# Kernel optimization log

Hardware: AMD Instinct MI355X
Metric: run time of the kernel (lower is better)

## Reference

```python
import jax, jax.numpy as jnp
import numpy as np

N_NODES = 50000
N_EDGES = 400000
H = 64          # node hidden state dim (entities_dimensions['node'])
E_DIM = 8       # edge_params dim (message.extra_parameters)
MSG_HID = 128   # message-creation MLP hidden width
RD_HID = 128    # readout hidden width
T = 2           # message-passing steps


def setup_inputs() -> dict:
    key = jax.random.key(0)
    ks = jax.random.split(key, 12)
    def w(k, shape):
        return jax.random.normal(k, shape, dtype=jnp.float32) * 0.05
    return {
        "node_feats": jax.random.normal(ks[0], (N_NODES, H), dtype=jnp.float32),
        "edge_feats": jax.random.normal(ks[1], (N_EDGES, E_DIM), dtype=jnp.float32),
        "edge_src": jax.random.randint(ks[2], (N_EDGES,), 0, N_NODES),
        "edge_dst": jax.random.randint(ks[3], (N_EDGES,), 0, N_NODES),
        # message creation MLP: concat(hs_src, hs_dst, edge_params) -> relu -> H
        "W_msg1": w(ks[4], (2 * H + E_DIM, MSG_HID)),
        "b_msg1": jnp.zeros((MSG_HID,), jnp.float32),
        "W_msg2": w(ks[5], (MSG_HID, H)),
        "b_msg2": jnp.zeros((H,), jnp.float32),
        # GRU cell update (keras GRUCell convention, reset_after=False)
        "W_x": w(ks[6], (H, 3 * H)),
        "W_h": w(ks[7], (H, 3 * H)),
        "b_gru": jnp.zeros((3 * H,), jnp.float32),
        # readout MLP: H -> relu -> 1
        "W_r1": w(ks[8], (H, RD_HID)),
        "b_r1": jnp.zeros((RD_HID,), jnp.float32),
        "W_r2": w(ks[9], (RD_HID, 1)),
        "b_r2": jnp.zeros((1,), jnp.float32),
    }


def _gru_cell(h, x, W_x, W_h, b):
    # gates order: update (z), reset (r), candidate (h~) — keras convention
    gx = x @ W_x + b
    gh = h @ W_h
    xz, xr, xh = jnp.split(gx, 3, axis=-1)
    hz, hr, hh = jnp.split(gh, 3, axis=-1)
    z = jax.nn.sigmoid(xz + hz)
    r = jax.nn.sigmoid(xr + hr)
    hc = jnp.tanh(xh + r * hh)
    return z * h + (1.0 - z) * hc


def reference(node_feats, edge_feats, edge_src, edge_dst,
              W_msg1, b_msg1, W_msg2, b_msg2,
              W_x, W_h, b_gru, W_r1, b_r1, W_r2, b_r2):
    h = node_feats  # [N, H] hidden states initialized from entity features
    for _ in range(T):
        # gather source/destination node states per edge: [E, H]
        src_h = h[edge_src]
        dst_h = h[edge_dst]
        m_in = jnp.concatenate([src_h, dst_h, edge_feats], axis=-1)  # [E, 2H+E_DIM]
        m = jax.nn.relu(m_in @ W_msg1 + b_msg1) @ W_msg2 + b_msg2    # [E, H]
        # scatter-sum aggregation to destination nodes: [N, H]
        agg = jax.ops.segment_sum(m, edge_dst, num_segments=N_NODES)
        # recurrent (GRU) node-state update
        h = _gru_cell(h, agg, W_x, W_h, b_gru)
    # readout MLP on final hidden states
    out = jax.nn.relu(h @ W_r1 + b_r1) @ W_r2 + b_r2  # [N, 1]
    return out
```

## Files before the change

kernel.cpp:

```cpp
#include <hip/hip_runtime.h>
#include <hip/hip_bf16.h>

#define NN 50000
#define NE 400000
#define NPAIR 12500
#define NCH 196
#define NPAD 50176

typedef __bf16 bf16_t;
typedef __bf16 bf16x4 __attribute__((ext_vector_type(4)));
typedef __bf16 bf16x8 __attribute__((ext_vector_type(8)));
typedef float  floatx4 __attribute__((ext_vector_type(4)));

static __device__ __forceinline__ floatx4 mfma16(bf16x8 a, bf16x8 b, floatx4 c) {
    return __builtin_amdgcn_mfma_f32_16x16x32_bf16(a, b, c, 0, 0, 0);
}
static __device__ __forceinline__ float sigm_f(float x) {
    return 1.f / (1.f + __expf(-x));
}
static __device__ __forceinline__ float tanh_f(float x) {
    return 1.f - 2.f / (__expf(2.f * x) + 1.f);
}
static __device__ __forceinline__ bf16x8 cvt8(const float* sp) {
    float4 f0 = *(const float4*)sp;
    float4 f1 = *(const float4*)(sp + 4);
    bf16x8 v;
    v[0] = (bf16_t)f0.x; v[1] = (bf16_t)f0.y; v[2] = (bf16_t)f0.z; v[3] = (bf16_t)f0.w;
    v[4] = (bf16_t)f1.x; v[5] = (bf16_t)f1.y; v[6] = (bf16_t)f1.z; v[7] = (bf16_t)f1.w;
    return v;
}

__global__ __launch_bounds__(256) void prep_kernel(
    const float* __restrict__ nf,
    const float* __restrict__ Wm1, const float* __restrict__ Wm2,
    const float* __restrict__ Wx,  const float* __restrict__ Wh,
    const float* __restrict__ Wr1,
    bf16_t* __restrict__ hb,
    bf16_t* __restrict__ W1f, bf16_t* __restrict__ W2f,
    bf16_t* __restrict__ Wxt, bf16_t* __restrict__ Wht,
    bf16_t* __restrict__ Wr1f)
{
    int u = blockIdx.x * 256 + threadIdx.x;
    if (u < 800000) {
        float4 v = *(const float4*)(nf + (size_t)u * 4);
        bf16x4 o;
        o[0] = (bf16_t)v.x; o[1] = (bf16_t)v.y; o[2] = (bf16_t)v.z; o[3] = (bf16_t)v.w;
        *(bf16x4*)(hb + (size_t)u * 4) = o;
        return;
    }
    u -= 800000;
    if (u < 20480) {
        int j = u & 7, l = (u >> 3) & 63, rem = u >> 9;
        int ks = rem % 5, nt = rem / 5;
        int n = nt * 16 + (l & 15);
        int k = ks * 32 + (l >> 4) * 8 + j;
        W1f[u] = (k < 136) ? (bf16_t)Wm1[k * 128 + n] : (bf16_t)0.f;
        return;
    }
    u -= 20480;
    if (u < 8192) {
        int j = u & 7, l = (u >> 3) & 63, rem = u >> 9;
        int kg = rem & 3, nt = rem >> 2;
        int n = nt * 16 + (l & 15);
        int k = kg * 32 + (l >> 4) * 8 + j;
        W2f[u] = (bf16_t)Wm2[k * 64 + n];
        return;
    }
    u -= 8192;
    if (u < 12288) {
        int n = u >> 6, k = u & 63;
        Wxt[u] = (bf16_t)Wx[k * 192 + n];
        return;
    }
    u -= 12288;
    if (u < 12288) {
        int n = u >> 6, k = u & 63;
        Wht[u] = (bf16_t)Wh[k * 192 + n];
        return;
    }
    u -= 12288;
    if (u < 8192) {
        int j = u & 7, l = (u >> 3) & 63, rem = u >> 9;
        int kg = rem & 1, nt = rem >> 1;
        int n = nt * 16 + (l & 15);
        int k = kg * 32 + (l >> 4) * 8 + j;
        Wr1f[u] = (bf16_t)Wr1[k * 128 + n];
    }
}

__global__ __launch_bounds__(256) void hist_kernel(
    const int* __restrict__ edst, int* __restrict__ deg)
{
    int e = blockIdx.x * 256 + threadIdx.x;
    if (e < NE) atomicAdd(&deg[edst[e]], 1);
}

__global__ __launch_bounds__(256) void scanA_kernel(
    const int* __restrict__ deg, int* __restrict__ chunkSums)
{
    __shared__ int s[256];
    int i = blockIdx.x * 256 + threadIdx.x;
    s[threadIdx.x] = deg[i];
    __syncthreads();
    for (int st = 128; st >= 1; st >>= 1) {
        if (threadIdx.x < st) s[threadIdx.x] += s[threadIdx.x + st];
        __syncthreads();
    }
    if (threadIdx.x == 0) chunkSums[blockIdx.x] = s[0];
}

__global__ __launch_bounds__(256) void scanB_kernel(
    const int* __restrict__ chunkSums, int* __restrict__ chunkOff)
{
    __shared__ int s[256];
    int t = threadIdx.x;
    int v = (t < NCH) ? chunkSums[t] : 0;
    s[t] = v;
    __syncthreads();
    for (int st = 1; st < 256; st <<= 1) {
        int add = (t >= st) ? s[t - st] : 0;
        __syncthreads();
        s[t] += add;
        __syncthreads();
    }
    if (t < NCH) chunkOff[t] = s[t] - v;
}

__global__ __launch_bounds__(256) void scanC_kernel(
    const int* __restrict__ deg, const int* __restrict__ chunkOff,
    int* __restrict__ cursor)
{
    __shared__ int s[256];
    int t = threadIdx.x;
    int i = blockIdx.x * 256 + t;
    int v = deg[i];
    s[t] = v;
    __syncthreads();
    for (int st = 1; st < 256; st <<= 1) {
        int add = (t >= st) ? s[t - st] : 0;
        __syncthreads();
        s[t] += add;
        __syncthreads();
    }
    cursor[i] = chunkOff[blockIdx.x] + s[t] - v;
}

__global__ __launch_bounds__(256) void scatter_kernel(
    const int* __restrict__ esrc, const int* __restrict__ edst,
    const float* __restrict__ ef,
    int* __restrict__ cursor, int* __restrict__ srcs, int* __restrict__ dsts,
    bf16_t* __restrict__ efpb)
{
    int e = blockIdx.x * 256 + threadIdx.x;
    if (e >= NE) return;
    int d = edst[e];
    int p = atomicAdd(&cursor[d], 1);
    srcs[p] = esrc[e];
    dsts[p] = d;
    float4 a = *(const float4*)(ef + (size_t)e * 8);
    float4 b = *(const float4*)(ef + (size_t)e * 8 + 4);
    bf16x8 v;
    v[0] = (bf16_t)a.x; v[1] = (bf16_t)a.y; v[2] = (bf16_t)a.z; v[3] = (bf16_t)a.w;
    v[4] = (bf16_t)b.x; v[5] = (bf16_t)b.y; v[6] = (bf16_t)b.z; v[7] = (bf16_t)b.w;
    *(bf16x8*)(efpb + (size_t)p * 8) = v;
}

__global__ __launch_bounds__(256) void edge_kernel(
    const bf16_t* __restrict__ hb, const bf16_t* __restrict__ efpb,
    const int* __restrict__ srcs, const int* __restrict__ dsts,
    const bf16_t* __restrict__ W1f, const bf16_t* __restrict__ W2f,
    const float* __restrict__ b1f, const float* __restrict__ b2f,
    bf16_t* __restrict__ mb)
{
    __shared__ __attribute__((aligned(16))) bf16_t w1s[20480];
    __shared__ __attribute__((aligned(16))) bf16_t w2s[8192];
    __shared__ __attribute__((aligned(16))) bf16_t hq[4][32 * 36];

    const int tid = threadIdx.x;
    {
        const uint4* s1 = (const uint4*)W1f;
        uint4* d1 = (uint4*)w1s;
        #pragma unroll
        for (int i = 0; i < 10; i++) d1[tid + i * 256] = s1[tid + i * 256];
        const uint4* s2 = (const uint4*)W2f;
        uint4* d2 = (uint4*)w2s;
        #pragma unroll
        for (int i = 0; i < 4; i++) d2[tid + i * 256] = s2[tid + i * 256];
    }
    __syncthreads();

    const int lane = tid & 63;
    const int wv   = tid >> 6;
    const int l15  = lane & 15;
    const int quad = lane >> 4;

    float b1r[8], b2r[4];
    #pragma unroll
    for (int nt = 0; nt < 8; nt++) b1r[nt] = b1f[nt * 16 + l15];
    #pragma unroll
    for (int nt = 0; nt < 4; nt++) b2r[nt] = b2f[nt * 16 + l15];

    const int WTOT = gridDim.x * 4;
    int p = blockIdx.x * 4 + wv;

    bf16x8 af0[5], af1[5];
    {
        int base = p * 32;
        int r0 = base + l15, r1 = base + 16 + l15;
        int si0 = srcs[r0], di0 = dsts[r0];
        int si1 = srcs[r1], di1 = dsts[r1];
        const bf16_t* sp0 = hb + (size_t)si0 * 64 + quad * 8;
        const bf16_t* dp0 = hb + (size_t)di0 * 64 + quad * 8;
        const bf16_t* sp1 = hb + (size_t)si1 * 64 + quad * 8;
        const bf16_t* dp1 = hb + (size_t)di1 * 64 + quad * 8;
        af0[0] = *(const bf16x8*)sp0;  af0[1] = *(const bf16x8*)(sp0 + 32);
        af0[2] = *(const bf16x8*)dp0;  af0[3] = *(const bf16x8*)(dp0 + 32);
        af1[0] = *(const bf16x8*)sp1;  af1[1] = *(const bf16x8*)(sp1 + 32);
        af1[2] = *(const bf16x8*)dp1;  af1[3] = *(const bf16x8*)(dp1 + 32);
        if (quad == 0) {
            af0[4] = *(const bf16x8*)(efpb + (size_t)r0 * 8);
            af1[4] = *(const bf16x8*)(efpb + (size_t)r1 * 8);
        } else {
            #pragma unroll
            for (int q = 0; q < 8; q++) { af0[4][q] = (bf16_t)0.f; af1[4][q] = (bf16_t)0.f; }
        }
    }

    while (true) {
        int pn = p + WTOT;
        int pp = (pn < NPAIR) ? pn : p;
        int nbase = pp * 32;
        int nr0 = nbase + l15, nr1 = nbase + 16 + l15;
        int si0n = srcs[nr0], di0n = dsts[nr0];
        int si1n = srcs[nr1], di1n = dsts[nr1];

        floatx4 oa0[4], oa1[4];
        #pragma unroll
        for (int nt = 0; nt < 4; nt++) {
            oa0[nt].x=0.f; oa0[nt].y=0.f; oa0[nt].z=0.f; oa0[nt].w=0.f;
            oa1[nt].x=0.f; oa1[nt].y=0.f; oa1[nt].z=0.f; oa1[nt].w=0.f;
        }

        #pragma unroll
        for (int q = 0; q < 4; q++) {
            floatx4 ac0[2], ac1[2];
            #pragma unroll
            for (int nt = 0; nt < 2; nt++) {
                ac0[nt].x=0.f; ac0[nt].y=0.f; ac0[nt].z=0.f; ac0[nt].w=0.f;
                ac1[nt].x=0.f; ac1[nt].y=0.f; ac1[nt].z=0.f; ac1[nt].w=0.f;
            }
            #pragma unroll
            for (int nt = 0; nt < 2; nt++) {
                int gnt = q * 2 + nt;
                #pragma unroll
                for (int ks = 0; ks < 5; ks++) {
                    bf16x8 b = *(const bf16x8*)(w1s + ((gnt * 5 + ks) * 64 + lane) * 8);
                    ac0[nt] = mfma16(af0[ks], b, ac0[nt]);
                    ac1[nt] = mfma16(af1[ks], b, ac1[nt]);
                }
            }
            #pragma unroll
            for (int nt = 0; nt < 2; nt++) {
                float bb = b1r[q * 2 + nt];
                #pragma unroll
                for (int r = 0; r < 4; r++) {
                    float v0 = fmaxf(ac0[nt][r] + bb, 0.f);
                    float v1 = fmaxf(ac1[nt][r] + bb, 0.f);
                    hq[wv][(quad * 4 + r) * 36 + nt * 16 + l15]      = (bf16_t)v0;
                    hq[wv][(16 + quad * 4 + r) * 36 + nt * 16 + l15] = (bf16_t)v1;
                }
            }
            bf16x8 hf0 = *(const bf16x8*)(hq[wv] + l15 * 36 + quad * 8);
            bf16x8 hf1 = *(const bf16x8*)(hq[wv] + (16 + l15) * 36 + quad * 8);
            #pragma unroll
            for (int nt = 0; nt < 4; nt++) {
                bf16x8 w2 = *(const bf16x8*)(w2s + ((nt * 4 + q) * 64 + lane) * 8);
                oa0[nt] = mfma16(hf0, w2, oa0[nt]);
                oa1[nt] = mfma16(hf1, w2, oa1[nt]);
            }
        }

        int base = p * 32;
        {
            const bf16_t* sp0 = hb + (size_t)si0n * 64 + quad * 8;
            const bf16_t* dp0 = hb + (size_t)di0n * 64 + quad * 8;
            const bf16_t* sp1 = hb + (size_t)si1n * 64 + quad * 8;
            const bf16_t* dp1 = hb + (size_t)di1n * 64 + quad * 8;
            af0[0] = *(const bf16x8*)sp0;  af0[1] = *(const bf16x8*)(sp0 + 32);
            af0[2] = *(const bf16x8*)dp0;  af0[3] = *(const bf16x8*)(dp0 + 32);
            af1[0] = *(const bf16x8*)sp1;  af1[1] = *(const bf16x8*)(sp1 + 32);
            af1[2] = *(const bf16x8*)dp1;  af1[3] = *(const bf16x8*)(dp1 + 32);
            if (quad == 0) {
                af0[4] = *(const bf16x8*)(efpb + (size_t)nr0 * 8);
                af1[4] = *(const bf16x8*)(efpb + (size_t)nr1 * 8);
            }
        }

        #pragma unroll
        for (int nt = 0; nt < 4; nt++) {
            int col = nt * 16 + l15;
            float bb = b2r[nt];
            #pragma unroll
            for (int r = 0; r < 4; r++) {
                int row0 = base + quad * 4 + r;
                int row1 = base + 16 + quad * 4 + r;
                mb[(size_t)row0 * 64 + col] = (bf16_t)(oa0[nt][r] + bb);
                mb[(size_t)row1 * 64 + col] = (bf16_t)(oa1[nt][r] + bb);
            }
        }

        if (pn >= NPAIR) break;
        p = pn;
    }
}

__global__ __launch_bounds__(256) void agg_kernel(
    const bf16_t* __restrict__ mb, const int* __restrict__ deg,
    const int* __restrict__ cursor, bf16_t* __restrict__ aggb)
{
    const int node = blockIdx.x * 4 + (threadIdx.x >> 6);
    if (node >= NN) return;
    const int lane = threadIdx.x & 63;
    int dg  = deg[node];
    int end = cursor[node];
    int st  = end - dg;
    float s0 = 0.f, s1 = 0.f;
    int e = st;
    for (; e + 1 < end; e += 2) {
        s0 += (float)mb[(size_t)e * 64 + lane];
        s1 += (float)mb[(size_t)(e + 1) * 64 + lane];
    }
    if (e < end) s0 += (float)mb[(size_t)e * 64 + lane];
    aggb[(size_t)node * 64 + lane] = (bf16_t)(s0 + s1);
}

template<int LAST>
__global__ __launch_bounds__(256) void gru_kernel(
    const bf16_t* __restrict__ aggb, const float* __restrict__ h_in,
    float* __restrict__ h_out, bf16_t* __restrict__ hb_out,
    const bf16_t* __restrict__ Wxt, const bf16_t* __restrict__ Wht,
    const float* __restrict__ bg,
    const bf16_t* __restrict__ Wr1f, const float* __restrict__ br1,
    const float* __restrict__ Wr2, const float* __restrict__ br2,
    float* __restrict__ out)
{
    __shared__ __attribute__((aligned(16))) float  shd[64 * 68];
    __shared__ __attribute__((aligned(16))) bf16_t hb2[4][16 * 72];
    const int tid = threadIdx.x;
    const int n0  = blockIdx.x * 64;

    for (int idx = tid; idx < 64 * 16; idx += 256) {
        int i = idx >> 4, c = (idx & 15) * 4;
        int n = n0 + i; if (n >= NN) n = NN - 1;
        *(float4*)&shd[i * 68 + c] = *(const float4*)(h_in + (size_t)n * 64 + c);
    }
    __syncthreads();

    const int lane = tid & 63;
    const int wv   = tid >> 6;
    const int l15  = lane & 15;
    const int quad = lane >> 4;
    const int rowA = wv * 16 + l15;
    int nA = n0 + rowA; if (nA >= NN) nA = NN - 1;

    bf16x8 ax[2], ah[2];
    ax[0] = *(const bf16x8*)(aggb + (size_t)nA * 64 + quad * 8);
    ax[1] = *(const bf16x8*)(aggb + (size_t)nA * 64 + quad * 8 + 32);
    {
        const float* hp = shd + rowA * 68 + quad * 8;
        ah[0] = cvt8(hp);
        ah[1] = cvt8(hp + 32);
    }

    floatx4 az[4], ar[4], axh[4], ahh[4];
    #pragma unroll
    for (int nt = 0; nt < 4; nt++) {
        az[nt].x=0.f; az[nt].y=0.f; az[nt].z=0.f; az[nt].w=0.f;
        ar[nt].x=0.f; ar[nt].y=0.f; ar[nt].z=0.f; ar[nt].w=0.f;
        axh[nt].x=0.f; axh[nt].y=0.f; axh[nt].z=0.f; axh[nt].w=0.f;
        ahh[nt].x=0.f; ahh[nt].y=0.f; ahh[nt].z=0.f; ahh[nt].w=0.f;
    }
    #pragma unroll
    for (int nt = 0; nt < 4; nt++) {
        const bf16_t* bx_z = Wxt + (nt * 16 + l15) * 64 + quad * 8;
        const bf16_t* bh_z = Wht + (nt * 16 + l15) * 64 + quad * 8;
        const bf16_t* bx_r = bx_z + 64 * 64;
        const bf16_t* bh_r = bh_z + 64 * 64;
        const bf16_t* bx_h = bx_z + 128 * 64;
        const bf16_t* bh_h = bh_z + 128 * 64;
        az[nt]  = mfma16(ax[0], *(const bf16x8*)bx_z,        az[nt]);
        az[nt]  = mfma16(ax[1], *(const bf16x8*)(bx_z + 32), az[nt]);
        az[nt]  = mfma16(ah[0], *(const bf16x8*)bh_z,        az[nt]);
        az[nt]  = mfma16(ah[1], *(const bf16x8*)(bh_z + 32), az[nt]);
        ar[nt]  = mfma16(ax[0], *(const bf16x8*)bx_r,        ar[nt]);
        ar[nt]  = mfma16(ax[1], *(const bf16x8*)(bx_r + 32), ar[nt]);
        ar[nt]  = mfma16(ah[0], *(const bf16x8*)bh_r,        ar[nt]);
        ar[nt]  = mfma16(ah[1], *(const bf16x8*)(bh_r + 32), ar[nt]);
        axh[nt] = mfma16(ax[0], *(const bf16x8*)bx_h,        axh[nt]);
        axh[nt] = mfma16(ax[1], *(const bf16x8*)(bx_h + 32), axh[nt]);
        ahh[nt] = mfma16(ah[0], *(const bf16x8*)bh_h,        ahh[nt]);
        ahh[nt] = mfma16(ah[1], *(const bf16x8*)(bh_h + 32), ahh[nt]);
    }

    #pragma unroll
    for (int nt = 0; nt < 4; nt++) {
        int j = nt * 16 + l15;
        float bz = bg[j], brr = bg[64 + j], bh = bg[128 + j];
        #pragma unroll
        for (int r = 0; r < 4; r++) {
            int lrow = wv * 16 + quad * 4 + r;
            int n = n0 + lrow;
            float z  = sigm_f(az[nt][r] + bz);
            float rr = sigm_f(ar[nt][r] + brr);
            float hc = tanh_f(axh[nt][r] + bh + rr * ahh[nt][r]);
            float hold = shd[lrow * 68 + j];
            float hnew = z * hold + (1.f - z) * hc;
            if (LAST) {
                hb2[wv][(quad * 4 + r) * 72 + j] = (bf16_t)hnew;
            } else if (n < NN) {
                h_out[(size_t)n * 64 + j]  = hnew;
                hb_out[(size_t)n * 64 + j] = (bf16_t)hnew;
            }
        }
    }

    if (LAST) {
        bf16x8 a0 = *(const bf16x8*)(hb2[wv] + l15 * 72 + quad * 8);
        bf16x8 a1 = *(const bf16x8*)(hb2[wv] + l15 * 72 + quad * 8 + 32);
        floatx4 accR[8];
        #pragma unroll
        for (int nt = 0; nt < 8; nt++) { accR[nt].x=0.f; accR[nt].y=0.f; accR[nt].z=0.f; accR[nt].w=0.f; }
        #pragma unroll
        for (int nt = 0; nt < 8; nt++) {
            bf16x8 b0 = *(const bf16x8*)(Wr1f + ((nt * 2 + 0) * 64 + lane) * 8);
            bf16x8 b1 = *(const bf16x8*)(Wr1f + ((nt * 2 + 1) * 64 + lane) * 8);
            accR[nt] = mfma16(a0, b0, accR[nt]);
            accR[nt] = mfma16(a1, b1, accR[nt]);
        }
        float br1r[8], wr2r[8];
        #pragma unroll
        for (int nt = 0; nt < 8; nt++) {
            br1r[nt] = br1[nt * 16 + l15];
            wr2r[nt] = Wr2[nt * 16 + l15];
        }
        float br2v = br2[0];
        #pragma unroll
        for (int r = 0; r < 4; r++) {
            float p = 0.f;
            #pragma unroll
            for (int nt = 0; nt < 8; nt++)
                p += fmaxf(accR[nt][r] + br1r[nt], 0.f) * wr2r[nt];
            p += __shfl_xor(p, 1, 64);
            p += __shfl_xor(p, 2, 64);
            p += __shfl_xor(p, 4, 64);
            p += __shfl_xor(p, 8, 64);
            if (l15 == 0) {
                int n = n0 + wv * 16 + quad * 4 + r;
                if (n < NN) out[n] = p + br2v;
            }
        }
    }
}

extern "C" void kernel_launch(void* const* d_in, const int* in_sizes, int n_in,
                              void* d_out, int out_size, void* d_ws, size_t ws_size,
                              hipStream_t stream)
{
    const float* nf  = (const float*)d_in[0];
    const float* ef  = (const float*)d_in[1];
    const int* esrc  = (const int*)d_in[2];
    const int* edst  = (const int*)d_in[3];
    const float* Wm1 = (const float*)d_in[4];
    const float* bm1 = (const float*)d_in[5];
    const float* Wm2 = (const float*)d_in[6];
    const float* bm2 = (const float*)d_in[7];
    const float* Wx  = (const float*)d_in[8];
    const float* Wh  = (const float*)d_in[9];
    const float* bg  = (const float*)d_in[10];
    const float* Wr1 = (const float*)d_in[11];
    const float* br1 = (const float*)d_in[12];
    const float* Wr2 = (const float*)d_in[13];
    const float* br2 = (const float*)d_in[14];

    char* ws = (char*)d_ws;
    float*  hbuf   = (float*)(ws);
    bf16_t* hb     = (bf16_t*)(ws + 12800000);
    bf16_t* W1f    = (bf16_t*)(ws + 19200000);
    bf16_t* W2f    = (bf16_t*)(ws + 19240960);
    bf16_t* Wxt    = (bf16_t*)(ws + 19257344);
    bf16_t* Wht    = (bf16_t*)(ws + 19281920);
    bf16_t* Wr1f   = (bf16_t*)(ws + 19306496);
    int*    srcs   = (int*)(ws + 19322880);
    int*    dsts   = (int*)(ws + 20922880);
    bf16_t* efpb   = (bf16_t*)(ws + 22522880);
    int*    deg    = (int*)(ws + 28922880);
    int*    cursor = (int*)(ws + 29123584);
    int*    chunkS = (int*)(ws + 29324288);
    int*    chunkO = (int*)(ws + 29325312);
    bf16_t* aggb   = (bf16_t*)(ws + 29326336);
    bf16_t* mb     = (bf16_t*)(ws + 35726336);

    prep_kernel<<<3365, 256, 0, stream>>>(nf, Wm1, Wm2, Wx, Wh, Wr1,
                                          hb, W1f, W2f, Wxt, Wht, Wr1f);

    hipMemsetAsync(deg, 0, (size_t)NPAD * 4, stream);
    hist_kernel<<<(NE + 255) / 256, 256, 0, stream>>>(edst, deg);
    scanA_kernel<<<NCH, 256, 0, stream>>>(deg, chunkS);
    scanB_kernel<<<1, 256, 0, stream>>>(chunkS, chunkO);
    scanC_kernel<<<NCH, 256, 0, stream>>>(deg, chunkO, cursor);
    scatter_kernel<<<(NE + 255) / 256, 256, 0, stream>>>(esrc, edst, ef, cursor,
                                                         srcs, dsts, efpb);

    edge_kernel<<<1024, 256, 0, stream>>>(hb, efpb, srcs, dsts,
                                          W1f, W2f, bm1, bm2, mb);
    agg_kernel<<<(NN + 3) / 4, 256, 0, stream>>>(mb, deg, cursor, aggb);
    gru_kernel<0><<<(NN + 63) / 64, 256, 0, stream>>>(
        aggb, nf, hbuf, hb, Wxt, Wht, bg, Wr1f, br1, Wr2, br2, (float*)d_out);
    edge_kernel<<<1024, 256, 0, stream>>>(hb, efpb, srcs, dsts,
                                          W1f, W2f, bm1, bm2, mb);
    agg_kernel<<<(NN + 3) / 4, 256, 0, stream>>>(mb, deg, cursor, aggb);
    gru_kernel<1><<<(NN + 63) / 64, 256, 0, stream>>>(
        aggb, hbuf, nullptr, nullptr, Wxt, Wht, bg, Wr1f, br1, Wr2, br2,
        (float*)d_out);
}
```

Baseline: 322.8 us.

## Fuse aggregation into GRU, merge histogram into prep, single-block scan

The segment-sum aggregation is folded into the GRU kernel: each lane sums its CSR segment of messages directly before the MFMA gate computation, which removes the agg kernel and the aggb round trip. The degree histogram now runs inside prep_kernel, and the three-kernel scan becomes one 1024-thread block, cutting launch count. The fp32 hidden-state buffer is dropped and step 2 reads the bf16 hidden state instead, which saves memory traffic but lowers precision. The fused aggregation loop runs per lane with a serial degree loop and may load-balance worse than the old one-wave-per-node agg kernel.

```diff
diff --git a/kernel.cpp b/kernel.cpp
--- a/kernel.cpp
+++ b/kernel.cpp
@@ -4,7 +4,6 @@
 #define NN 50000
 #define NE 400000
 #define NPAIR 12500
-#define NCH 196
 #define NPAD 50176
 
 typedef __bf16 bf16_t;
@@ -34,11 +33,11 @@
     const float* __restrict__ nf,
     const float* __restrict__ Wm1, const float* __restrict__ Wm2,
     const float* __restrict__ Wx,  const float* __restrict__ Wh,
-    const float* __restrict__ Wr1,
+    const float* __restrict__ Wr1, const int* __restrict__ edst,
     bf16_t* __restrict__ hb,
     bf16_t* __restrict__ W1f, bf16_t* __restrict__ W2f,
     bf16_t* __restrict__ Wxt, bf16_t* __restrict__ Wht,
-    bf16_t* __restrict__ Wr1f)
+    bf16_t* __restrict__ Wr1f, int* __restrict__ deg)
 {
     int u = blockIdx.x * 256 + threadIdx.x;
     if (u < 800000) {
@@ -85,64 +84,36 @@
         int n = nt * 16 + (l & 15);
         int k = kg * 32 + (l >> 4) * 8 + j;
         Wr1f[u] = (bf16_t)Wr1[k * 128 + n];
-    }
-}
-
-__global__ __launch_bounds__(256) void hist_kernel(
-    const int* __restrict__ edst, int* __restrict__ deg)
-{
-    int e = blockIdx.x * 256 + threadIdx.x;
-    if (e < NE) atomicAdd(&deg[edst[e]], 1);
-}
-
-__global__ __launch_bounds__(256) void scanA_kernel(
-    const int* __restrict__ deg, int* __restrict__ chunkSums)
-{
-    __shared__ int s[256];
-    int i = blockIdx.x * 256 + threadIdx.x;
-    s[threadIdx.x] = deg[i];
+        return;
+    }
+    u -= 8192;
+    if (u < NE) atomicAdd(&deg[edst[u]], 1);
+}
+
+__global__ __launch_bounds__(1024) void scan_kernel(
+    const int* __restrict__ deg, int* __restrict__ cursor)
+{
+    __shared__ int part[1024];
+    const int t = threadIdx.x;
+    const int base = t * 49;
+    int sum = 0;
+    #pragma unroll 1
+    for (int i = 0; i < 49; i++) sum += deg[base + i];
+    part[t] = sum;
     __syncthreads();
-    for (int st = 128; st >= 1; st >>= 1) {
-        if (threadIdx.x < st) s[threadIdx.x] += s[threadIdx.x + st];
+    for (int st = 1; st < 1024; st <<= 1) {
+        int add = (t >= st) ? part[t - st] : 0;
         __syncthreads();
-    }
-    if (threadIdx.x == 0) chunkSums[blockIdx.x] = s[0];
-}
-
-__global__ __launch_bounds__(256) void scanB_kernel(
-    const int* __restrict__ chunkSums, int* __restrict__ chunkOff)
-{
-    __shared__ int s[256];
-    int t = threadIdx.x;
-    int v = (t < NCH) ? chunkSums[t] : 0;
-    s[t] = v;
-    __syncthreads();
-    for (int st = 1; st < 256; st <<= 1) {
-        int add = (t >= st) ? s[t - st] : 0;
+        part[t] += add;
         __syncthreads();
-        s[t] += add;
-        __syncthreads();
-    }
-    if (t < NCH) chunkOff[t] = s[t] - v;
-}
-
-__global__ __launch_bounds__(256) void scanC_kernel(
-    const int* __restrict__ deg, const int* __restrict__ chunkOff,
-    int* __restrict__ cursor)
-{
-    __shared__ int s[256];
-    int t = threadIdx.x;
-    int i = blockIdx.x * 256 + t;
-    int v = deg[i];
-    s[t] = v;
-    __syncthreads();
-    for (int st = 1; st < 256; st <<= 1) {
-        int add = (t >= st) ? s[t - st] : 0;
-        __syncthreads();
-        s[t] += add;
-        __syncthreads();
-    }
-    cursor[i] = chunkOff[blockIdx.x] + s[t] - v;
+    }
+    int run = part[t] - sum;
+    #pragma unroll 1
+    for (int i = 0; i < 49; i++) {
+        int d = deg[base + i];
+        cursor[base + i] = run;
+        run += d;
+    }
 }
 
 __global__ __launch_bounds__(256) void scatter_kernel(
@@ -314,30 +285,12 @@
     }
 }
 
-__global__ __launch_bounds__(256) void agg_kernel(
-    const bf16_t* __restrict__ mb, const int* __restrict__ deg,
-    const int* __restrict__ cursor, bf16_t* __restrict__ aggb)
-{
-    const int node = blockIdx.x * 4 + (threadIdx.x >> 6);
-    if (node >= NN) return;
-    const int lane = threadIdx.x & 63;
-    int dg  = deg[node];
-    int end = cursor[node];
-    int st  = end - dg;
-    float s0 = 0.f, s1 = 0.f;
-    int e = st;
-    for (; e + 1 < end; e += 2) {
-        s0 += (float)mb[(size_t)e * 64 + lane];
-        s1 += (float)mb[(size_t)(e + 1) * 64 + lane];
-    }
-    if (e < end) s0 += (float)mb[(size_t)e * 64 + lane];
-    aggb[(size_t)node * 64 + lane] = (bf16_t)(s0 + s1);
-}
-
 template<int LAST>
 __global__ __launch_bounds__(256) void gru_kernel(
-    const bf16_t* __restrict__ aggb, const float* __restrict__ h_in,
-    float* __restrict__ h_out, bf16_t* __restrict__ hb_out,
+    const bf16_t* __restrict__ mb, const int* __restrict__ deg,
+    const int* __restrict__ cursor,
+    const float* __restrict__ hf, const bf16_t* __restrict__ hbin,
+    bf16_t* __restrict__ hb_out,
     const bf16_t* __restrict__ Wxt, const bf16_t* __restrict__ Wht,
     const float* __restrict__ bg,
     const bf16_t* __restrict__ Wr1f, const float* __restrict__ br1,
@@ -352,7 +305,15 @@
     for (int idx = tid; idx < 64 * 16; idx += 256) {
         int i = idx >> 4, c = (idx & 15) * 4;
         int n = n0 + i; if (n >= NN) n = NN - 1;
-        *(float4*)&shd[i * 68 + c] = *(const float4*)(h_in + (size_t)n * 64 + c);
+        if (LAST == 0) {
+            *(float4*)&shd[i * 68 + c] = *(const float4*)(hf + (size_t)n * 64 + c);
+        } else {
+            bf16x4 v = *(const bf16x4*)(hbin + (size_t)n * 64 + c);
+            shd[i * 68 + c + 0] = (float)v[0];
+            shd[i * 68 + c + 1] = (float)v[1];
+            shd[i * 68 + c + 2] = (float)v[2];
+            shd[i * 68 + c + 3] = (float)v[3];
+        }
     }
     __syncthreads();
 
@@ -363,9 +324,31 @@
     const int rowA = wv * 16 + l15;
     int nA = n0 + rowA; if (nA >= NN) nA = NN - 1;
 
-    bf16x8 ax[2], ah[2];
-    ax[0] = *(const bf16x8*)(aggb + (size_t)nA * 64 + quad * 8);
-    ax[1] = *(const bf16x8*)(aggb + (size_t)nA * 64 + quad * 8 + 32);
+    bf16x8 ax[2];
+    {
+        int en = cursor[nA];
+        int st = en - deg[nA];
+        float fa0[8], fa1[8];
+        #pragma unroll
+        for (int j = 0; j < 8; j++) { fa0[j] = 0.f; fa1[j] = 0.f; }
+        #pragma unroll 1
+        for (int e = st; e < en; e++) {
+            bf16x8 v0 = *(const bf16x8*)(mb + (size_t)e * 64 + quad * 8);
+            bf16x8 v1 = *(const bf16x8*)(mb + (size_t)e * 64 + 32 + quad * 8);
+            #pragma unroll
+            for (int j = 0; j < 8; j++) {
+                fa0[j] += (float)v0[j];
+                fa1[j] += (float)v1[j];
+            }
+        }
+        #pragma unroll
+        for (int j = 0; j < 8; j++) {
+            ax[0][j] = (bf16_t)fa0[j];
+            ax[1][j] = (bf16_t)fa1[j];
+        }
+    }
+
+    bf16x8 ah[2];
     {
         const float* hp = shd + rowA * 68 + quad * 8;
         ah[0] = cvt8(hp);
@@ -418,7 +401,6 @@
             if (LAST) {
                 hb2[wv][(quad * 4 + r) * 72 + j] = (bf16_t)hnew;
             } else if (n < NN) {
-                h_out[(size_t)n * 64 + j]  = hnew;
                 hb_out[(size_t)n * 64 + j] = (bf16_t)hnew;
             }
         }
@@ -483,43 +465,33 @@
     const float* br2 = (const float*)d_in[14];
 
     char* ws = (char*)d_ws;
-    float*  hbuf   = (float*)(ws);
-    bf16_t* hb     = (bf16_t*)(ws + 12800000);
-    bf16_t* W1f    = (bf16_t*)(ws + 19200000);
-    bf16_t* W2f    = (bf16_t*)(ws + 19240960);
-    bf16_t* Wxt    = (bf16_t*)(ws + 19257344);
-    bf16_t* Wht    = (bf16_t*)(ws + 19281920);
-    bf16_t* Wr1f   = (bf16_t*)(ws + 19306496);
-    int*    srcs   = (int*)(ws + 19322880);
-    int*    dsts   = (int*)(ws + 20922880);
-    bf16_t* efpb   = (bf16_t*)(ws + 22522880);
-    int*    deg    = (int*)(ws + 28922880);
-    int*    cursor = (int*)(ws + 29123584);
-    int*    chunkS = (int*)(ws + 29324288);
-    int*    chunkO = (int*)(ws + 29325312);
-    bf16_t* aggb   = (bf16_t*)(ws + 29326336);
-    bf16_t* mb     = (bf16_t*)(ws + 35726336);
-
-    prep_kernel<<<3365, 256, 0, stream>>>(nf, Wm1, Wm2, Wx, Wh, Wr1,
-                                          hb, W1f, W2f, Wxt, Wht, Wr1f);
+    bf16_t* hb     = (bf16_t*)(ws);
+    bf16_t* W1f    = (bf16_t*)(ws + 6400000);
+    bf16_t* W2f    = (bf16_t*)(ws + 6440960);
+    bf16_t* Wxt    = (bf16_t*)(ws + 6457344);
+    bf16_t* Wht    = (bf16_t*)(ws + 6481920);
+    bf16_t* Wr1f   = (bf16_t*)(ws + 6506496);
+    int*    srcs   = (int*)(ws + 6522880);
+    int*    dsts   = (int*)(ws + 8122880);
+    bf16_t* efpb   = (bf16_t*)(ws + 9722880);
+    int*    deg    = (int*)(ws + 16122880);
+    int*    cursor = (int*)(ws + 16323584);
+    bf16_t* mb     = (bf16_t*)(ws + 16524288);
 
     hipMemsetAsync(deg, 0, (size_t)NPAD * 4, stream);
-    hist_kernel<<<(NE + 255) / 256, 256, 0, stream>>>(edst, deg);
-    scanA_kernel<<<NCH, 256, 0, stream>>>(deg, chunkS);
-    scanB_kernel<<<1, 256, 0, stream>>>(chunkS, chunkO);
-    scanC_kernel<<<NCH, 256, 0, stream>>>(deg, chunkO, cursor);
+    prep_kernel<<<4928, 256, 0, stream>>>(nf, Wm1, Wm2, Wx, Wh, Wr1, edst,
+                                          hb, W1f, W2f, Wxt, Wht, Wr1f, deg);
+    scan_kernel<<<1, 1024, 0, stream>>>(deg, cursor);
     scatter_kernel<<<(NE + 255) / 256, 256, 0, stream>>>(esrc, edst, ef, cursor,
                                                          srcs, dsts, efpb);
-
     edge_kernel<<<1024, 256, 0, stream>>>(hb, efpb, srcs, dsts,
                                           W1f, W2f, bm1, bm2, mb);
-    agg_kernel<<<(NN + 3) / 4, 256, 0, stream>>>(mb, deg, cursor, aggb);
     gru_kernel<0><<<(NN + 63) / 64, 256, 0, stream>>>(
-        aggb, nf, hbuf, hb, Wxt, Wht, bg, Wr1f, br1, Wr2, br2, (float*)d_out);
+        mb, deg, cursor, nf, nullptr, hb,
+        Wxt, Wht, bg, Wr1f, br1, Wr2, br2, (float*)d_out);
     edge_kernel<<<1024, 256, 0, stream>>>(hb, efpb, srcs, dsts,
                                           W1f, W2f, bm1, bm2, mb);
-    agg_kernel<<<(NN + 3) / 4, 256, 0, stream>>>(mb, deg, cursor, aggb);
     gru_kernel<1><<<(NN + 63) / 64, 256, 0, stream>>>(
-        aggb, hbuf, nullptr, nullptr, Wxt, Wht, bg, Wr1f, br1, Wr2, br2,
-        (float*)d_out);
-}
+        mb, deg, cursor, nullptr, hb, nullptr,
+        Wxt, Wht, bg, Wr1f, br1, Wr2, br2, (float*)d_out);
+}
```

Result: slower. 369.8 us (+14.6%).
